# Kernel tuning notes

Measured on AMD Instinct MI355X. Metric: run time of the kernel, lower is better.

The kernel has to match this reference:

```python
import jax, jax.numpy as jnp
import numpy as np

D_H, D_G, D_PROJ = 1280, 768, 256
SCALE = D_PROJ ** (-0.5)

def setup_inputs() -> dict:
    key = jax.random.key(0)
    k1, k2, k3, k4 = jax.random.split(key, 4)
    B, L, T = 8, 4096, 512
    H = jax.random.normal(k1, (B, L, D_H), dtype=jnp.float32)
    G = jax.random.normal(k2, (B, T, D_G), dtype=jnp.float32)
    attn_mask = jnp.zeros((B, L), dtype=bool)  # True = pad/ignore
    # nn.Linear weights: (out_features, in_features)
    Wk = jax.random.normal(k3, (D_PROJ, D_H), dtype=jnp.float32) * (D_H ** -0.5)
    Wq = jax.random.normal(k4, (D_PROJ, D_G), dtype=jnp.float32) * (D_G ** -0.5)
    return {"H": H, "G": G, "attn_mask": attn_mask, "Wk": Wk, "Wq": Wq}

def reference(H, G, attn_mask, Wk, Wq):
    # K = Wk(H): (B,L,P); Q = Wq(G): (B,T,P)
    K = jnp.einsum('bld,pd->blp', H, Wk)
    Q = jnp.einsum('btd,pd->btp', G, Wq)
    # scores (B,T,L); streaming two-pass softmax in the original is exactly
    # softmax over L -> compute it stably in one fused expression here.
    logits = jnp.einsum('btp,blp->btl', Q, K) * SCALE
    logits = jnp.where(attn_mask[:, None, :], -jnp.inf, logits)
    alpha = jax.nn.softmax(logits, axis=-1)
    Z = jnp.einsum('btl,bld->btd', alpha, H)  # (B,T,Dh)
    return Z
```

## Files before the change

kernel.cpp:

```cpp
#include <hip/hip_runtime.h>
#include <hip/hip_bf16.h>
#include <stdint.h>


typedef float f32x4 __attribute__((ext_vector_type(4)));
typedef short bf16x8 __attribute__((ext_vector_type(8)));

__device__ __forceinline__ unsigned short f2bf(float f) {
    __hip_bfloat16 h = __float2bfloat16(f);
    return __builtin_bit_cast(unsigned short, h);
}
__device__ __forceinline__ float bf2f(unsigned short h) {
    union { uint32_t u; float f; } v; v.u = ((uint32_t)h) << 16;
    return v.f;
}

__device__ __forceinline__ int xcdswz(int bx, int nbx) {
    int cpx = nbx >> 3;
    return (bx & 7) * cpx + (bx >> 3);
}

__device__ __forceinline__ void gload16(const unsigned short* g, unsigned short* l) {
    __builtin_amdgcn_global_load_lds(
        (const __attribute__((address_space(1))) void*)g,
        (__attribute__((address_space(3))) void*)l,
        16, 0, 0);
}

__device__ __forceinline__ int lidx(int row, int kshort) {
    return row * 40 + (((kshort >> 3) ^ ((row >> 3) & 3)) << 3) + (kshort & 7);
}

template<bool AF32, bool BF32, bool OBF16, bool TNF>
__global__ __launch_bounds__(256)
void gemm_bt(const void* __restrict__ Ap, const void* __restrict__ Bp,
             void* __restrict__ Cp, int M, int N, int K,
             long sA, long sB, long sC, float scale)
{
    __shared__ __align__(16) unsigned short lA[128 * 40];
    __shared__ __align__(16) unsigned short lB[128 * 40];

    const int bx = xcdswz(blockIdx.x, gridDim.x);
    const int mt = M >> 7, nt = N >> 7;
    const int tm = TNF ? (bx / nt) : (bx % mt);
    const int tn = TNF ? (bx % nt) : (bx / mt);
    const int b  = blockIdx.y;
    const int tid = threadIdx.x;
    const int lane = tid & 63, wv = tid >> 6;
    const int wr = wv >> 1, wc = wv & 1;
    const int fr = lane & 15, fk = lane >> 4;

    f32x4 acc[4][4] = {};

    const char* Abase = (const char*)Ap;
    const char* Bbase = (const char*)Bp;

    for (int k0 = 0; k0 < K; k0 += 32) {
        if constexpr (AF32) {
            const float* A = (const float*)Abase + (long)b * sA + (long)tm * 128 * K + k0;
            #pragma unroll
            for (int it = 0; it < 4; ++it) {
                int chunk = it * 256 + tid;
                int row = chunk >> 3;
                int kc  = (chunk & 7) << 2;
                const float4 v = *(const float4*)(A + (long)row * K + kc);
                ushort4 w;
                w.x = f2bf(v.x); w.y = f2bf(v.y); w.z = f2bf(v.z); w.w = f2bf(v.w);
                *(ushort4*)(&lA[lidx(row, kc)]) = w;
            }
        } else {
            const unsigned short* A = (const unsigned short*)Abase + (long)b * sA + (long)tm * 128 * K + k0;
            #pragma unroll
            for (int it = 0; it < 2; ++it) {
                int chunk = it * 256 + tid;
                int row = chunk >> 2;
                int kc  = (chunk & 3) << 3;
                *(uint4*)(&lA[lidx(row, kc)]) = *(const uint4*)(A + (long)row * K + kc);
            }
        }
        if constexpr (BF32) {
            const float* B = (const float*)Bbase + (long)b * sB + (long)tn * 128 * K + k0;
            #pragma unroll
            for (int it = 0; it < 4; ++it) {
                int chunk = it * 256 + tid;
                int row = chunk >> 3;
                int kc  = (chunk & 7) << 2;
                const float4 v = *(const float4*)(B + (long)row * K + kc);
                ushort4 w;
                w.x = f2bf(v.x); w.y = f2bf(v.y); w.z = f2bf(v.z); w.w = f2bf(v.w);
                *(ushort4*)(&lB[lidx(row, kc)]) = w;
            }
        } else {
            const unsigned short* B = (const unsigned short*)Bbase + (long)b * sB + (long)tn * 128 * K + k0;
            #pragma unroll
            for (int it = 0; it < 2; ++it) {
                int chunk = it * 256 + tid;
                int row = chunk >> 2;
                int kc  = (chunk & 3) << 3;
                *(uint4*)(&lB[lidx(row, kc)]) = *(const uint4*)(B + (long)row * K + kc);
            }
        }
        __syncthreads();
        bf16x8 af[4], bfr[4];
        #pragma unroll
        for (int i = 0; i < 4; ++i)
            af[i] = *(const bf16x8*)(&lA[lidx(wr * 64 + i * 16 + fr, fk * 8)]);
        #pragma unroll
        for (int i = 0; i < 4; ++i)
            bfr[i] = *(const bf16x8*)(&lB[lidx(wc * 64 + i * 16 + fr, fk * 8)]);
        #pragma unroll
        for (int mi = 0; mi < 4; ++mi)
            #pragma unroll
            for (int ni = 0; ni < 4; ++ni)
                acc[mi][ni] = __builtin_amdgcn_mfma_f32_16x16x32_bf16(af[mi], bfr[ni], acc[mi][ni], 0, 0, 0);
        __syncthreads();
    }

    if constexpr (OBF16) {
        unsigned short* C = (unsigned short*)Cp + (long)b * sC + ((long)tm * 128) * N + (long)tn * 128;
        #pragma unroll
        for (int mi = 0; mi < 4; ++mi)
            #pragma unroll
            for (int ni = 0; ni < 4; ++ni)
                #pragma unroll
                for (int j = 0; j < 4; ++j) {
                    int m = wr * 64 + mi * 16 + fk * 4 + j;
                    int n = wc * 64 + ni * 16 + fr;
                    C[(long)m * N + n] = f2bf(acc[mi][ni][j] * scale);
                }
    } else {
        float* C = (float*)Cp + (long)b * sC + ((long)tm * 128) * N + (long)tn * 128;
        #pragma unroll
        for (int mi = 0; mi < 4; ++mi)
            #pragma unroll
            for (int ni = 0; ni < 4; ++ni)
                #pragma unroll
                for (int j = 0; j < 4; ++j) {
                    int m = wr * 64 + mi * 16 + fk * 4 + j;
                    int n = wc * 64 + ni * 16 + fr;
                    C[(long)m * N + n] = acc[mi][ni][j] * scale;
                }
    }
}

template<int TN, bool OBF16>
__global__ __launch_bounds__(256)
void gemm_bt16(const unsigned short* __restrict__ Ap, const unsigned short* __restrict__ Bp,
               void* __restrict__ Cp, int M, int N, int K,
               long sA, long sB, long sC, float scale)
{
    constexpr int NB = TN / 32;
    constexpr int BISS = TN / 64;
    __shared__ __align__(16) unsigned short lA[128 * 32];
    __shared__ __align__(16) unsigned short lB[TN * 32];

    const int bx = xcdswz(blockIdx.x, gridDim.x);
    const int mt = M >> 7;
    const int tm = bx % mt, tn = bx / mt;
    const int b  = blockIdx.y;
    const int tid = threadIdx.x;
    const int lane = tid & 63, wv = tid >> 6;
    const int wr = wv >> 1, wc = wv & 1;
    const int fr = lane & 15, fk = lane >> 4;

    f32x4 acc[4][NB] = {};

    const unsigned short* A0 = Ap + (long)b * sA + (long)tm * 128 * K;
    const unsigned short* B0 = Bp + (long)b * sB + (long)tn * TN * K;

    for (int k0 = 0; k0 < K; k0 += 32) {
        #pragma unroll
        for (int q = 0; q < 2; ++q) {
            int slot = wv * 128 + q * 64 + lane;
            int row = slot >> 2, kc = (slot & 3) << 3;
            gload16(A0 + (long)row * K + k0 + kc, lA + (size_t)(wv * 128 + q * 64) * 8);
        }
        #pragma unroll
        for (int q = 0; q < BISS; ++q) {
            int slot = wv * (BISS * 64) + q * 64 + lane;
            int row = slot >> 2, kc = (slot & 3) << 3;
            gload16(B0 + (long)row * K + k0 + kc, lB + (size_t)(wv * (BISS * 64) + q * 64) * 8);
        }
        __syncthreads();
        bf16x8 af[4], bfv[NB];
        #pragma unroll
        for (int i = 0; i < 4; ++i)
            af[i] = *(const bf16x8*)(lA + (wr * 64 + i * 16 + fr) * 32 + fk * 8);
        #pragma unroll
        for (int i = 0; i < NB; ++i)
            bfv[i] = *(const bf16x8*)(lB + (wc * (TN / 2) + i * 16 + fr) * 32 + fk * 8);
        #pragma unroll
        for (int mi = 0; mi < 4; ++mi)
            #pragma unroll
            for (int ni = 0; ni < NB; ++ni)
                acc[mi][ni] = __builtin_amdgcn_mfma_f32_16x16x32_bf16(af[mi], bfv[ni], acc[mi][ni], 0, 0, 0);
        __syncthreads();
    }

    if constexpr (OBF16) {
        unsigned short* C = (unsigned short*)Cp + (long)b * sC + ((long)tm * 128) * N + (long)tn * TN;
        #pragma unroll
        for (int mi = 0; mi < 4; ++mi)
            #pragma unroll
            for (int ni = 0; ni < NB; ++ni)
                #pragma unroll
                for (int j = 0; j < 4; ++j) {
                    int m = wr * 64 + mi * 16 + fk * 4 + j;
                    int n = wc * (TN / 2) + ni * 16 + fr;
                    C[(long)m * N + n] = f2bf(acc[mi][ni][j] * scale);
                }
    } else {
        float* C = (float*)Cp + (long)b * sC + ((long)tm * 128) * N + (long)tn * TN;
        #pragma unroll
        for (int mi = 0; mi < 4; ++mi)
            #pragma unroll
            for (int ni = 0; ni < NB; ++ni)
                #pragma unroll
                for (int j = 0; j < 4; ++j) {
                    int m = wr * 64 + mi * 16 + fk * 4 + j;
                    int n = wc * (TN / 2) + ni * 16 + fr;
                    C[(long)m * N + n] = acc[mi][ni][j] * scale;
                }
    }
}

__global__ __launch_bounds__(256)
void transpose_h(const float* __restrict__ H, unsigned short* __restrict__ Hbt)
{
    __shared__ unsigned short lT[64 * 72];
    const int ntile = 64 * 20 * 8;
    for (int tileid = blockIdx.x; tileid < ntile; tileid += gridDim.x) {
        int tmp = tileid;
        const int dt = tmp % 20; tmp /= 20;
        const int lt = tmp % 64;
        const int b  = tmp / 64;
        const int l0 = lt * 64, d0 = dt * 64;
        const float* Hs = H + ((long)b * 4096 + l0) * 1280 + d0;
        #pragma unroll
        for (int it = 0; it < 4; ++it) {
            int chunk = it * 256 + threadIdx.x;
            int lr = chunk >> 4, dc4 = (chunk & 15) << 2;
            float4 v = *(const float4*)(Hs + (long)lr * 1280 + dc4);
            unsigned short w[4] = { f2bf(v.x), f2bf(v.y), f2bf(v.z), f2bf(v.w) };
            #pragma unroll
            for (int j = 0; j < 4; ++j) {
                int d = dc4 + j;
                int sl = (lr & 15) | ((((lr >> 4) ^ (d >> 2)) & 3) << 4);
                lT[d * 72 + sl] = w[j];
            }
        }
        __syncthreads();
        {
            int drow = threadIdx.x >> 2, lc = threadIdx.x & 3;
            int slc = lc ^ ((drow >> 2) & 3);
            const uint4* src = (const uint4*)(lT + drow * 72 + slc * 16);
            unsigned short* dst = Hbt + ((long)b * 1280 + d0 + drow) * 4096 + l0 + lc * 16;
            uint4 v0 = src[0], v1 = src[1];
            *(uint4*)(dst)     = v0;
            *(uint4*)(dst + 8) = v1;
        }
        __syncthreads();
    }
}

__global__ __launch_bounds__(256)
void gemm_kn(const unsigned short* __restrict__ Ap, const float* __restrict__ Bp,
             float* __restrict__ Cp, int M, int N, int K,
             long sA, long sB, long sC)
{
    __shared__ __align__(16) unsigned short lA[128 * 40];
    __shared__ __align__(16) unsigned short lB[64 * 40];

    const int bx = xcdswz(blockIdx.x, gridDim.x);
    const int mt = M >> 7;
    const int tm = bx % mt;
    const int tn = bx / mt;
    const int b  = blockIdx.y;
    const int tid = threadIdx.x;
    const int lane = tid & 63, wv = tid >> 6;
    const int wr = wv >> 1, wc = wv & 1;
    const int fr = lane & 15, fk = lane >> 4;

    f32x4 acc[4][2] = {};

    const unsigned short* A0 = Ap + (long)b * sA + (long)tm * 128 * K;
    const int nn    = tid & 63;
    const int khalf = tid >> 6;

    for (int k0 = 0; k0 < K; k0 += 32) {
        #pragma unroll
        for (int it = 0; it < 2; ++it) {
            int chunk = it * 256 + tid;
            int row = chunk >> 2;
            int kc  = (chunk & 3) << 3;
            *(uint4*)(&lA[lidx(row, kc)]) = *(const uint4*)(A0 + (long)row * K + k0 + kc);
        }
        {
            const float* Bb = Bp + (long)b * sB + (long)(k0 + khalf * 8) * N + (long)tn * 64 + nn;
            unsigned short t8[8];
            #pragma unroll
            for (int kk = 0; kk < 8; ++kk)
                t8[kk] = f2bf(Bb[(long)kk * N]);
            *(uint4*)(&lB[lidx(nn, khalf * 8)]) = *(uint4*)(&t8[0]);
        }
        __syncthreads();
        bf16x8 af[4], bfr[2];
        #pragma unroll
        for (int i = 0; i < 4; ++i)
            af[i] = *(const bf16x8*)(&lA[lidx(wr * 64 + i * 16 + fr, fk * 8)]);
        #pragma unroll
        for (int i = 0; i < 2; ++i)
            bfr[i] = *(const bf16x8*)(&lB[lidx(wc * 32 + i * 16 + fr, fk * 8)]);
        #pragma unroll
        for (int mi = 0; mi < 4; ++mi)
            #pragma unroll
            for (int ni = 0; ni < 2; ++ni)
                acc[mi][ni] = __builtin_amdgcn_mfma_f32_16x16x32_bf16(af[mi], bfr[ni], acc[mi][ni], 0, 0, 0);
        __syncthreads();
    }

    float* C = Cp + (long)b * sC + ((long)tm * 128) * N + (long)tn * 64;
    #pragma unroll
    for (int mi = 0; mi < 4; ++mi)
        #pragma unroll
        for (int ni = 0; ni < 2; ++ni)
            #pragma unroll
            for (int j = 0; j < 4; ++j) {
                int m = wr * 64 + mi * 16 + fk * 4 + j;
                int n = wc * 32 + ni * 16 + fr;
                C[(long)m * N + n] = acc[mi][ni][j];
            }
}

__global__ __launch_bounds__(256)
void softmax_rows(unsigned short* __restrict__ S, const unsigned char* __restrict__ mask)
{
    const int row = blockIdx.x;
    const int b = row >> 9;
    const long base = (long)row * 4096;
    const int tid = threadIdx.x, lane = tid & 63, wv = tid >> 6;
    __shared__ float red[8];

    uint4 s0 = *(const uint4*)(S + base + tid * 16);
    uint4 s1 = *(const uint4*)(S + base + tid * 16 + 8);
    uint4 mv = *(const uint4*)(mask + (long)b * 4096 + tid * 16);
    const unsigned char* mb = (const unsigned char*)&mv;

    unsigned int words[8] = { s0.x, s0.y, s0.z, s0.w, s1.x, s1.y, s1.z, s1.w };
    float x[16];
    #pragma unroll
    for (int i = 0; i < 8; ++i) {
        x[2 * i]     = bf2f((unsigned short)(words[i] & 0xffffu));
        x[2 * i + 1] = bf2f((unsigned short)(words[i] >> 16));
    }
    #pragma unroll
    for (int i = 0; i < 16; ++i)
        if (mb[i]) x[i] = -1e30f;

    float m = x[0];
    #pragma unroll
    for (int i = 1; i < 16; ++i) m = fmaxf(m, x[i]);
    #pragma unroll
    for (int off = 32; off; off >>= 1) m = fmaxf(m, __shfl_xor(m, off));
    if (lane == 0) red[wv] = m;
    __syncthreads();
    m = fmaxf(fmaxf(red[0], red[1]), fmaxf(red[2], red[3]));

    float p[16];
    float s = 0.f;
    #pragma unroll
    for (int i = 0; i < 16; ++i) { p[i] = __expf(x[i] - m); s += p[i]; }
    #pragma unroll
    for (int off = 32; off; off >>= 1) s += __shfl_xor(s, off);
    if (lane == 0) red[4 + wv] = s;
    __syncthreads();
    s = (red[4] + red[5]) + (red[6] + red[7]);
    const float inv = 1.0f / s;

    unsigned int ow[8];
    #pragma unroll
    for (int i = 0; i < 8; ++i) {
        unsigned int lo = f2bf(p[2 * i] * inv);
        unsigned int hi = f2bf(p[2 * i + 1] * inv);
        ow[i] = lo | (hi << 16);
    }
    uint4 o0 = { ow[0], ow[1], ow[2], ow[3] };
    uint4 o1 = { ow[4], ow[5], ow[6], ow[7] };
    *(uint4*)(S + base + tid * 16)     = o0;
    *(uint4*)(S + base + tid * 16 + 8) = o1;
}

extern "C" void kernel_launch(void* const* d_in, const int* in_sizes, int n_in,
                              void* d_out, int out_size, void* d_ws, size_t ws_size,
                              hipStream_t stream)
{
    const float*         H    = (const float*)d_in[0];
    const float*         G    = (const float*)d_in[1];
    const unsigned char* mask = (const unsigned char*)d_in[2];
    const float*         Wk   = (const float*)d_in[3];
    const float*         Wq   = (const float*)d_in[4];
    float*               out  = (float*)d_out;

    const long nK = (long)8 * 4096 * 256;
    const long nQ = (long)8 * 512 * 256;
    const long nS = (long)8 * 512 * 4096;
    const long nH = (long)8 * 1280 * 4096;

    unsigned short* Kb  = (unsigned short*)d_ws;
    unsigned short* Qb  = Kb + nK;
    unsigned short* Sb  = Qb + nQ;
    unsigned short* Hbt = Sb + nS;
    const bool big = ws_size >= (size_t)(nK + nQ + nS + nH) * 2;

    gemm_bt<true, true, true, true><<<dim3(512, 1), 256, 0, stream>>>(
        H, Wk, Kb, 32768, 256, 1280, 0, 0, 0, 1.0f);
    gemm_bt<true, true, true, true><<<dim3(64, 1), 256, 0, stream>>>(
        G, Wq, Qb, 4096, 256, 768, 0, 0, 0, 1.0f);

    if (big) {
        transpose_h<<<dim3(2048), 256, 0, stream>>>(H, Hbt);
        gemm_bt16<128, true><<<dim3(128, 8), 256, 0, stream>>>(
            Qb, Kb, Sb, 512, 4096, 256,
            (long)512 * 256, (long)4096 * 256, (long)512 * 4096, 0.0625f);
        softmax_rows<<<dim3(4096), 256, 0, stream>>>(Sb, mask);
        gemm_bt16<64, false><<<dim3(80, 8), 256, 0, stream>>>(
            Sb, Hbt, out, 512, 1280, 4096,
            (long)512 * 4096, (long)1280 * 4096, (long)512 * 1280, 1.0f);
    } else {
        gemm_bt<false, false, true, false><<<dim3(128, 8), 256, 0, stream>>>(
            Qb, Kb, Sb, 512, 4096, 256,
            (long)512 * 256, (long)4096 * 256, (long)512 * 4096, 0.0625f);
        softmax_rows<<<dim3(4096), 256, 0, stream>>>(Sb, mask);
        gemm_kn<<<dim3(80, 8), 256, 0, stream>>>(
            Sb, H, out, 512, 1280, 4096,
            (long)512 * 4096, (long)4096 * 1280, (long)512 * 1280);
    }
}
```

Measured before the change: 279.7 us.

## Rewrite score and output GEMMs with swizzled LDS tiles and split-K waves

The QK^T score GEMM now uses a dedicated kernel with a K-step of 64 and an XOR-swizzled LDS layout, loaded by direct global-to-LDS copies. The final alpha·H GEMM is replaced by a kernel that gives each of its four waves a different K slice of a 128x64 tile over a K-step of 128, then reduces the partial sums through LDS. The generic GEMM template is also trimmed to the fp32-input path. The aim is fewer barriers per unit of work and fewer LDS bank conflicts. The cost is larger LDS footprints, a serialized cross-wave reduction, and only one wave writing the output.

```diff
diff --git a/kernel.cpp b/kernel.cpp
--- a/kernel.cpp
+++ b/kernel.cpp
@@ -31,11 +31,10 @@
     return row * 40 + (((kshort >> 3) ^ ((row >> 3) & 3)) << 3) + (kshort & 7);
 }
 
-template<bool AF32, bool BF32, bool OBF16, bool TNF>
-__global__ __launch_bounds__(256)
-void gemm_bt(const void* __restrict__ Ap, const void* __restrict__ Bp,
-             void* __restrict__ Cp, int M, int N, int K,
-             long sA, long sB, long sC, float scale)
+template<bool TNF>
+__global__ __launch_bounds__(256)
+void gemm_bt(const float* __restrict__ Ap, const float* __restrict__ Bp,
+             unsigned short* __restrict__ Cp, int M, int N, int K)
 {
     __shared__ __align__(16) unsigned short lA[128 * 40];
     __shared__ __align__(16) unsigned short lB[128 * 40];
@@ -44,7 +43,6 @@
     const int mt = M >> 7, nt = N >> 7;
     const int tm = TNF ? (bx / nt) : (bx % mt);
     const int tn = TNF ? (bx % nt) : (bx / mt);
-    const int b  = blockIdx.y;
     const int tid = threadIdx.x;
     const int lane = tid & 63, wv = tid >> 6;
     const int wr = wv >> 1, wc = wv & 1;
@@ -52,12 +50,9 @@
 
     f32x4 acc[4][4] = {};
 
-    const char* Abase = (const char*)Ap;
-    const char* Bbase = (const char*)Bp;
-
     for (int k0 = 0; k0 < K; k0 += 32) {
-        if constexpr (AF32) {
-            const float* A = (const float*)Abase + (long)b * sA + (long)tm * 128 * K + k0;
+        {
+            const float* A = Ap + (long)tm * 128 * K + k0;
             #pragma unroll
             for (int it = 0; it < 4; ++it) {
                 int chunk = it * 256 + tid;
@@ -68,18 +63,9 @@
                 w.x = f2bf(v.x); w.y = f2bf(v.y); w.z = f2bf(v.z); w.w = f2bf(v.w);
                 *(ushort4*)(&lA[lidx(row, kc)]) = w;
             }
-        } else {
-            const unsigned short* A = (const unsigned short*)Abase + (long)b * sA + (long)tm * 128 * K + k0;
-            #pragma unroll
-            for (int it = 0; it < 2; ++it) {
-                int chunk = it * 256 + tid;
-                int row = chunk >> 2;
-                int kc  = (chunk & 3) << 3;
-                *(uint4*)(&lA[lidx(row, kc)]) = *(const uint4*)(A + (long)row * K + kc);
-            }
-        }
-        if constexpr (BF32) {
-            const float* B = (const float*)Bbase + (long)b * sB + (long)tn * 128 * K + k0;
+        }
+        {
+            const float* B = Bp + (long)tn * 128 * K + k0;
             #pragma unroll
             for (int it = 0; it < 4; ++it) {
                 int chunk = it * 256 + tid;
@@ -90,15 +76,6 @@
                 w.x = f2bf(v.x); w.y = f2bf(v.y); w.z = f2bf(v.z); w.w = f2bf(v.w);
                 *(ushort4*)(&lB[lidx(row, kc)]) = w;
             }
-        } else {
-            const unsigned short* B = (const unsigned short*)Bbase + (long)b * sB + (long)tn * 128 * K + k0;
-            #pragma unroll
-            for (int it = 0; it < 2; ++it) {
-                int chunk = it * 256 + tid;
-                int row = chunk >> 2;
-                int kc  = (chunk & 3) << 3;
-                *(uint4*)(&lB[lidx(row, kc)]) = *(const uint4*)(B + (long)row * K + kc);
-            }
         }
         __syncthreads();
         bf16x8 af[4], bfr[4];
@@ -116,43 +93,26 @@
         __syncthreads();
     }
 
-    if constexpr (OBF16) {
-        unsigned short* C = (unsigned short*)Cp + (long)b * sC + ((long)tm * 128) * N + (long)tn * 128;
-        #pragma unroll
-        for (int mi = 0; mi < 4; ++mi)
-            #pragma unroll
-            for (int ni = 0; ni < 4; ++ni)
-                #pragma unroll
-                for (int j = 0; j < 4; ++j) {
-                    int m = wr * 64 + mi * 16 + fk * 4 + j;
-                    int n = wc * 64 + ni * 16 + fr;
-                    C[(long)m * N + n] = f2bf(acc[mi][ni][j] * scale);
-                }
-    } else {
-        float* C = (float*)Cp + (long)b * sC + ((long)tm * 128) * N + (long)tn * 128;
-        #pragma unroll
-        for (int mi = 0; mi < 4; ++mi)
-            #pragma unroll
-            for (int ni = 0; ni < 4; ++ni)
-                #pragma unroll
-                for (int j = 0; j < 4; ++j) {
-                    int m = wr * 64 + mi * 16 + fk * 4 + j;
-                    int n = wc * 64 + ni * 16 + fr;
-                    C[(long)m * N + n] = acc[mi][ni][j] * scale;
-                }
-    }
-}
-
-template<int TN, bool OBF16>
-__global__ __launch_bounds__(256)
-void gemm_bt16(const unsigned short* __restrict__ Ap, const unsigned short* __restrict__ Bp,
-               void* __restrict__ Cp, int M, int N, int K,
-               long sA, long sB, long sC, float scale)
-{
-    constexpr int NB = TN / 32;
-    constexpr int BISS = TN / 64;
-    __shared__ __align__(16) unsigned short lA[128 * 32];
-    __shared__ __align__(16) unsigned short lB[TN * 32];
+    unsigned short* C = Cp + ((long)tm * 128) * N + (long)tn * 128;
+    #pragma unroll
+    for (int mi = 0; mi < 4; ++mi)
+        #pragma unroll
+        for (int ni = 0; ni < 4; ++ni)
+            #pragma unroll
+            for (int j = 0; j < 4; ++j) {
+                int m = wr * 64 + mi * 16 + fk * 4 + j;
+                int n = wc * 64 + ni * 16 + fr;
+                C[(long)m * N + n] = f2bf(acc[mi][ni][j]);
+            }
+}
+
+__global__ __launch_bounds__(256)
+void gemm_bt16s(const unsigned short* __restrict__ Ap, const unsigned short* __restrict__ Bp,
+                unsigned short* __restrict__ Cp, int M, int N, int K,
+                long sA, long sB, long sC, float scale)
+{
+    __shared__ __align__(16) unsigned short lA[128 * 64];
+    __shared__ __align__(16) unsigned short lB[128 * 64];
 
     const int bx = xcdswz(blockIdx.x, gridDim.x);
     const int mt = M >> 7;
@@ -163,64 +123,137 @@
     const int wr = wv >> 1, wc = wv & 1;
     const int fr = lane & 15, fk = lane >> 4;
 
-    f32x4 acc[4][NB] = {};
+    f32x4 acc[4][4] = {};
 
     const unsigned short* A0 = Ap + (long)b * sA + (long)tm * 128 * K;
-    const unsigned short* B0 = Bp + (long)b * sB + (long)tn * TN * K;
-
-    for (int k0 = 0; k0 < K; k0 += 32) {
-        #pragma unroll
-        for (int q = 0; q < 2; ++q) {
-            int slot = wv * 128 + q * 64 + lane;
-            int row = slot >> 2, kc = (slot & 3) << 3;
-            gload16(A0 + (long)row * K + k0 + kc, lA + (size_t)(wv * 128 + q * 64) * 8);
-        }
-        #pragma unroll
-        for (int q = 0; q < BISS; ++q) {
-            int slot = wv * (BISS * 64) + q * 64 + lane;
-            int row = slot >> 2, kc = (slot & 3) << 3;
-            gload16(B0 + (long)row * K + k0 + kc, lB + (size_t)(wv * (BISS * 64) + q * 64) * 8);
-        }
-        __syncthreads();
-        bf16x8 af[4], bfv[NB];
+    const unsigned short* B0 = Bp + (long)b * sB + (long)tn * 128 * K;
+
+    for (int k0 = 0; k0 < K; k0 += 64) {
+        #pragma unroll
+        for (int q = 0; q < 4; ++q) {
+            int slot = wv * 256 + q * 64 + lane;
+            int row = slot >> 3, c = slot & 7;
+            int ks = (c ^ (row & 7)) << 3;
+            gload16(A0 + (long)row * K + k0 + ks, lA + (size_t)(wv * 256 + q * 64) * 8);
+            gload16(B0 + (long)row * K + k0 + ks, lB + (size_t)(wv * 256 + q * 64) * 8);
+        }
+        __syncthreads();
+        bf16x8 af[2][4], bfv[2][4];
+        #pragma unroll
+        for (int ks = 0; ks < 2; ++ks) {
+            int csw = ((ks * 4 + fk) ^ (fr & 7)) << 3;
+            #pragma unroll
+            for (int i = 0; i < 4; ++i) {
+                af[ks][i]  = *(const bf16x8*)(lA + (wr * 64 + i * 16 + fr) * 64 + csw);
+                bfv[ks][i] = *(const bf16x8*)(lB + (wc * 64 + i * 16 + fr) * 64 + csw);
+            }
+        }
+        #pragma unroll
+        for (int mi = 0; mi < 4; ++mi)
+            #pragma unroll
+            for (int ni = 0; ni < 4; ++ni)
+                #pragma unroll
+                for (int ks = 0; ks < 2; ++ks)
+                    acc[mi][ni] = __builtin_amdgcn_mfma_f32_16x16x32_bf16(af[ks][mi], bfv[ks][ni], acc[mi][ni], 0, 0, 0);
+        __syncthreads();
+    }
+
+    unsigned short* C = Cp + (long)b * sC + ((long)tm * 128) * N + (long)tn * 128;
+    #pragma unroll
+    for (int mi = 0; mi < 4; ++mi)
+        #pragma unroll
+        for (int ni = 0; ni < 4; ++ni)
+            #pragma unroll
+            for (int j = 0; j < 4; ++j) {
+                int m = wr * 64 + mi * 16 + fk * 4 + j;
+                int n = wc * 64 + ni * 16 + fr;
+                C[(long)m * N + n] = f2bf(acc[mi][ni][j] * scale);
+            }
+}
+
+__global__ __launch_bounds__(256)
+void zk(const unsigned short* __restrict__ Sb, const unsigned short* __restrict__ Hbt,
+        float* __restrict__ out)
+{
+    __shared__ __align__(16) unsigned short lA[128 * 128];
+    __shared__ __align__(16) unsigned short lB[64 * 128];
+
+    const int K = 4096, N = 1280;
+    const int bx = xcdswz(blockIdx.x, gridDim.x);
+    const int tm = bx & 3, tn = bx >> 2;
+    const int b  = blockIdx.y;
+    const int tid = threadIdx.x;
+    const int lane = tid & 63, wv = tid >> 6;
+    const int fr = lane & 15, fk = lane >> 4;
+
+    f32x4 acc[8][4] = {};
+
+    const unsigned short* A0 = Sb  + ((long)b * 512  + tm * 128) * K;
+    const unsigned short* B0 = Hbt + ((long)b * 1280 + tn * 64) * K;
+
+    for (int k0 = 0; k0 < K; k0 += 128) {
+        #pragma unroll
+        for (int q = 0; q < 8; ++q) {
+            int slot = wv * 512 + q * 64 + lane;
+            int row = slot >> 4, c = slot & 15;
+            gload16(A0 + (long)row * K + k0 + ((c ^ (row & 7)) << 3),
+                    lA + (size_t)(wv * 512 + q * 64) * 8);
+        }
+        #pragma unroll
+        for (int q = 0; q < 4; ++q) {
+            int slot = wv * 256 + q * 64 + lane;
+            int row = slot >> 4, c = slot & 15;
+            gload16(B0 + (long)row * K + k0 + ((c ^ (row & 7)) << 3),
+                    lB + (size_t)(wv * 256 + q * 64) * 8);
+        }
+        __syncthreads();
+        const int csw = ((wv * 4 + fk) ^ (fr & 7)) << 3;
+        bf16x8 bfv[4];
         #pragma unroll
         for (int i = 0; i < 4; ++i)
-            af[i] = *(const bf16x8*)(lA + (wr * 64 + i * 16 + fr) * 32 + fk * 8);
-        #pragma unroll
-        for (int i = 0; i < NB; ++i)
-            bfv[i] = *(const bf16x8*)(lB + (wc * (TN / 2) + i * 16 + fr) * 32 + fk * 8);
-        #pragma unroll
-        for (int mi = 0; mi < 4; ++mi)
-            #pragma unroll
-            for (int ni = 0; ni < NB; ++ni)
-                acc[mi][ni] = __builtin_amdgcn_mfma_f32_16x16x32_bf16(af[mi], bfv[ni], acc[mi][ni], 0, 0, 0);
-        __syncthreads();
-    }
-
-    if constexpr (OBF16) {
-        unsigned short* C = (unsigned short*)Cp + (long)b * sC + ((long)tm * 128) * N + (long)tn * TN;
-        #pragma unroll
-        for (int mi = 0; mi < 4; ++mi)
-            #pragma unroll
-            for (int ni = 0; ni < NB; ++ni)
+            bfv[i] = *(const bf16x8*)(lB + (i * 16 + fr) * 128 + csw);
+        #pragma unroll
+        for (int mi = 0; mi < 8; ++mi) {
+            bf16x8 af = *(const bf16x8*)(lA + (mi * 16 + fr) * 128 + csw);
+            #pragma unroll
+            for (int ni = 0; ni < 4; ++ni)
+                acc[mi][ni] = __builtin_amdgcn_mfma_f32_16x16x32_bf16(af, bfv[ni], acc[mi][ni], 0, 0, 0);
+        }
+        __syncthreads();
+    }
+
+    f32x4* red = (f32x4*)lA;
+    #pragma unroll 1
+    for (int w = 1; w < 4; ++w) {
+        __syncthreads();
+        if (wv == w) {
+            #pragma unroll
+            for (int mi = 0; mi < 8; ++mi)
                 #pragma unroll
-                for (int j = 0; j < 4; ++j) {
-                    int m = wr * 64 + mi * 16 + fk * 4 + j;
-                    int n = wc * (TN / 2) + ni * 16 + fr;
-                    C[(long)m * N + n] = f2bf(acc[mi][ni][j] * scale);
+                for (int ni = 0; ni < 4; ++ni)
+                    red[(mi * 4 + ni) * 64 + lane] = acc[mi][ni];
+        }
+        __syncthreads();
+        if (wv == 0) {
+            #pragma unroll
+            for (int mi = 0; mi < 8; ++mi)
+                #pragma unroll
+                for (int ni = 0; ni < 4; ++ni) {
+                    f32x4 v = red[(mi * 4 + ni) * 64 + lane];
+                    acc[mi][ni][0] += v[0]; acc[mi][ni][1] += v[1];
+                    acc[mi][ni][2] += v[2]; acc[mi][ni][3] += v[3];
                 }
-    } else {
-        float* C = (float*)Cp + (long)b * sC + ((long)tm * 128) * N + (long)tn * TN;
-        #pragma unroll
-        for (int mi = 0; mi < 4; ++mi)
-            #pragma unroll
-            for (int ni = 0; ni < NB; ++ni)
+        }
+    }
+    if (wv == 0) {
+        float* C = out + ((long)b * 512 + tm * 128) * N + tn * 64;
+        #pragma unroll
+        for (int mi = 0; mi < 8; ++mi)
+            #pragma unroll
+            for (int ni = 0; ni < 4; ++ni)
                 #pragma unroll
-                for (int j = 0; j < 4; ++j) {
-                    int m = wr * 64 + mi * 16 + fk * 4 + j;
-                    int n = wc * (TN / 2) + ni * 16 + fr;
-                    C[(long)m * N + n] = acc[mi][ni][j] * scale;
-                }
+                for (int j = 0; j < 4; ++j)
+                    C[(long)(mi * 16 + fk * 4 + j) * N + ni * 16 + fr] = acc[mi][ni][j];
     }
 }
 
@@ -412,22 +445,18 @@
     unsigned short* Hbt = Sb + nS;
     const bool big = ws_size >= (size_t)(nK + nQ + nS + nH) * 2;
 
-    gemm_bt<true, true, true, true><<<dim3(512, 1), 256, 0, stream>>>(
-        H, Wk, Kb, 32768, 256, 1280, 0, 0, 0, 1.0f);
-    gemm_bt<true, true, true, true><<<dim3(64, 1), 256, 0, stream>>>(
-        G, Wq, Qb, 4096, 256, 768, 0, 0, 0, 1.0f);
+    gemm_bt<true><<<dim3(512, 1), 256, 0, stream>>>(H, Wk, Kb, 32768, 256, 1280);
+    gemm_bt<true><<<dim3(64, 1), 256, 0, stream>>>(G, Wq, Qb, 4096, 256, 768);
 
     if (big) {
         transpose_h<<<dim3(2048), 256, 0, stream>>>(H, Hbt);
-        gemm_bt16<128, true><<<dim3(128, 8), 256, 0, stream>>>(
+        gemm_bt16s<<<dim3(128, 8), 256, 0, stream>>>(
             Qb, Kb, Sb, 512, 4096, 256,
             (long)512 * 256, (long)4096 * 256, (long)512 * 4096, 0.0625f);
         softmax_rows<<<dim3(4096), 256, 0, stream>>>(Sb, mask);
-        gemm_bt16<64, false><<<dim3(80, 8), 256, 0, stream>>>(
-            Sb, Hbt, out, 512, 1280, 4096,
-            (long)512 * 4096, (long)1280 * 4096, (long)512 * 1280, 1.0f);
+        zk<<<dim3(80, 8), 256, 0, stream>>>(Sb, Hbt, out);
     } else {
-        gemm_bt<false, false, true, false><<<dim3(128, 8), 256, 0, stream>>>(
+        gemm_bt16s<<<dim3(128, 8), 256, 0, stream>>>(
             Qb, Kb, Sb, 512, 4096, 256,
             (long)512 * 256, (long)4096 * 256, (long)512 * 4096, 0.0625f);
         softmax_rows<<<dim3(4096), 256, 0, stream>>>(Sb, mask);
```

New measurement: 330.2 us. 1.18x slower.
